# Kernel tuning notes

Hardware: AMD Instinct MI355X
Metric: run time of the kernel (lower is better)

Reference implementation:

```python
import jax, jax.numpy as jnp
import numpy as np

N = 100000      # nodes
F_IN = 500      # input features
HEADS = 8
HID = 8         # per-head hidden channels
NC = 16         # num classes
E = 1600000     # edges (avg degree 16)


def setup_inputs() -> dict:
    key = jax.random.key(0)
    ks = jax.random.split(key, 12)
    s = 0.1
    return {
        "x": jax.random.normal(ks[0], (N, F_IN), jnp.float32),
        "edge_index": jax.random.randint(ks[1], (2, E), 0, N, dtype=jnp.int64),
        "W1": jax.random.normal(ks[2], (F_IN, HEADS * HID), jnp.float32) * s,
        "a1_src": jax.random.normal(ks[3], (HEADS, HID), jnp.float32) * s,
        "a1_dst": jax.random.normal(ks[4], (HEADS, HID), jnp.float32) * s,
        "b1": jnp.zeros((HEADS * HID,), jnp.float32),
        "W2": jax.random.normal(ks[5], (HEADS * HID, NC), jnp.float32) * s,
        "a2_src": jax.random.normal(ks[6], (1, NC), jnp.float32) * s,
        "a2_dst": jax.random.normal(ks[7], (1, NC), jnp.float32) * s,
        "b2": jnp.zeros((NC,), jnp.float32),
        "Wg": jax.random.normal(ks[8], (NC, NC), jnp.float32) * s,
        "bg": jnp.zeros((NC,), jnp.float32),
    }


def _gat_layer(x, src, dst, W, a_src, a_dst, b, heads, ch):
    # PyG GATConv (eval mode): per-edge additive attention + scatter softmax.
    n = x.shape[0]
    h = (x @ W).reshape(n, heads, ch)                       # [N,H,C]
    al_s = jnp.einsum('nhc,hc->nh', h, a_src)               # [N,H]
    al_d = jnp.einsum('nhc,hc->nh', h, a_dst)
    e = jax.nn.leaky_relu(al_s[src] + al_d[dst], 0.2)       # [Etot,H]
    e_max = jax.ops.segment_max(e, dst, num_segments=n)     # stable softmax per dst
    ex = jnp.exp(e - e_max[dst])
    denom = jax.ops.segment_sum(ex, dst, num_segments=n)
    alpha = ex / (denom[dst] + 1e-16)                       # [Etot,H]
    out = jax.ops.segment_sum(alpha[:, :, None] * h[src], dst, num_segments=n)
    return out.reshape(n, heads * ch) + b


def _gcn_layer(x, src, dst, W, b):
    n = x.shape[0]
    deg = jax.ops.segment_sum(jnp.ones_like(dst, x.dtype), dst, num_segments=n)
    dinv = jnp.where(deg > 0, jax.lax.rsqrt(deg), 0.0)
    norm = dinv[src] * dinv[dst]                            # [Etot]
    xw = x @ W
    return jax.ops.segment_sum(norm[:, None] * xw[src], dst, num_segments=n) + b


def reference(x, edge_index, W1, a1_src, a1_dst, b1, W2, a2_src, a2_dst, b2, Wg, bg):
    n = x.shape[0]
    loop = jnp.arange(n, dtype=edge_index.dtype)
    src = jnp.concatenate([edge_index[0], loop])            # add self-loops (PyG default)
    dst = jnp.concatenate([edge_index[1], loop])
    # GAT: dropout layers are eval-mode no-ops
    h = jax.nn.elu(_gat_layer(x, src, dst, W1, a1_src, a1_dst, b1, HEADS, HID))
    h = _gat_layer(h, src, dst, W2, a2_src, a2_dst, b2, 1, NC)
    h = jax.nn.relu(h)                                      # activate='relu'
    return _gcn_layer(h, src, dst, Wg, bg)
```

## Files before the change

### kernel.cpp

```cpp
#include <hip/hip_runtime.h>
#include <hip/hip_bf16.h>
#include <math.h>

#define NNODES 100000
#define F_IN   500
#define HEADS  8
#define HID    8
#define NC     16

__global__ void zero_int_kernel(int* __restrict__ p, int n) {
    int i = blockIdx.x * blockDim.x + threadIdx.x;
    if (i < n) p[i] = 0;
}

__global__ void deg_kernel(const int* __restrict__ ei_dst, int* __restrict__ deg,
                           int E, int N) {
    int e = blockIdx.x * blockDim.x + threadIdx.x;
    int tot = E + N;
    if (e >= tot) return;
    int d = (e < E) ? ei_dst[e] : (e - E);
    atomicAdd(&deg[d], 1);
}

__global__ void scan1_kernel(const int* __restrict__ deg, int* __restrict__ bsum, int n) {
    __shared__ int s[256];
    int i = blockIdx.x * 256 + threadIdx.x;
    s[threadIdx.x] = (i < n) ? deg[i] : 0;
    __syncthreads();
    for (int off = 128; off > 0; off >>= 1) {
        if (threadIdx.x < off) s[threadIdx.x] += s[threadIdx.x + off];
        __syncthreads();
    }
    if (threadIdx.x == 0) bsum[blockIdx.x] = s[0];
}

__global__ void scan2_kernel(const int* __restrict__ bsum, int* __restrict__ bexcl, int nb) {
    __shared__ int s[512];
    int t = threadIdx.x;
    int orig = (t < nb) ? bsum[t] : 0;
    s[t] = orig;
    __syncthreads();
    for (int off = 1; off < 512; off <<= 1) {
        int v = (t >= off) ? s[t - off] : 0;
        __syncthreads();
        s[t] += v;
        __syncthreads();
    }
    if (t < nb) bexcl[t] = s[t] - orig;
}

__global__ void scan3_kernel(const int* __restrict__ deg, const int* __restrict__ bexcl,
                             int* __restrict__ rowptr, int n) {
    __shared__ int s[256];
    int t = threadIdx.x;
    int i = blockIdx.x * 256 + t;
    int v = (i < n) ? deg[i] : 0;
    s[t] = v;
    __syncthreads();
    for (int off = 1; off < 256; off <<= 1) {
        int u = (t >= off) ? s[t - off] : 0;
        __syncthreads();
        s[t] += u;
        __syncthreads();
    }
    if (i < n) rowptr[i + 1] = bexcl[blockIdx.x] + s[t];
    if (i == 0) rowptr[0] = 0;
}

__global__ void fill_kernel(const int* __restrict__ ei_src, const int* __restrict__ ei_dst,
                            const int* __restrict__ rowptr, int* __restrict__ cursor,
                            int* __restrict__ col, int E, int N) {
    int e = blockIdx.x * blockDim.x + threadIdx.x;
    int tot = E + N;
    if (e >= tot) return;
    int s, d;
    if (e < E) { s = ei_src[e]; d = ei_dst[e]; }
    else       { s = e - E;     d = s; }
    int pos = atomicAdd(&cursor[d], 1);
    col[rowptr[d] + pos] = s;
}

__global__ __launch_bounds__(256) void gemm1_kernel(const float* __restrict__ x,
                                                    const float* __restrict__ W,
                                                    float* __restrict__ h, int n) {
    __shared__ float xs[64][20];
    __shared__ float ws[20][64];
    int row0 = blockIdx.x * 64;
    int t = threadIdx.x;
    int ty = t >> 4, tx = t & 15;
    float acc[4][4] = {};
    for (int k0 = 0; k0 < F_IN; k0 += 20) {
#pragma unroll
        for (int i = 0; i < 5; ++i) {
            int f = t + i * 256;
            int r = f / 20, c = f - r * 20;
            int gr = row0 + r;
            xs[r][c] = (gr < n) ? x[(size_t)gr * F_IN + k0 + c] : 0.f;
        }
#pragma unroll
        for (int i = 0; i < 5; ++i) {
            int f = t + i * 256;
            int r = f >> 6, c = f & 63;
            ws[r][c] = W[(k0 + r) * 64 + c];
        }
        __syncthreads();
#pragma unroll
        for (int k = 0; k < 20; ++k) {
            float a[4], b[4];
#pragma unroll
            for (int i = 0; i < 4; ++i) a[i] = xs[ty * 4 + i][k];
#pragma unroll
            for (int j = 0; j < 4; ++j) b[j] = ws[k][tx * 4 + j];
#pragma unroll
            for (int i = 0; i < 4; ++i)
#pragma unroll
                for (int j = 0; j < 4; ++j) acc[i][j] += a[i] * b[j];
        }
        __syncthreads();
    }
#pragma unroll
    for (int i = 0; i < 4; ++i) {
        int gr = row0 + ty * 4 + i;
        if (gr < n) {
            float4 v = make_float4(acc[i][0], acc[i][1], acc[i][2], acc[i][3]);
            *reinterpret_cast<float4*>(h + (size_t)gr * 64 + tx * 4) = v;
        }
    }
}

__global__ void proj_al1_kernel(const float* __restrict__ h, const float* __restrict__ a1s,
                                const float* __restrict__ a1d, float* __restrict__ als,
                                float* __restrict__ ald, int n) {
    int nid = blockIdx.x * blockDim.x + threadIdx.x;
    if (nid >= n) return;
    const float* hp = h + (size_t)nid * 64;
#pragma unroll
    for (int hd = 0; hd < 8; ++hd) {
        float s = 0.f, d = 0.f;
#pragma unroll
        for (int c = 0; c < 8; ++c) {
            float hv = hp[hd * 8 + c];
            s += hv * a1s[hd * 8 + c];
            d += hv * a1d[hd * 8 + c];
        }
        als[nid * 8 + hd] = s;
        ald[nid * 8 + hd] = d;
    }
}

__global__ void gat1_edge_kernel(const int* __restrict__ rowptr, const int* __restrict__ col,
                                 const float* __restrict__ als, const float* __restrict__ ald,
                                 const float* __restrict__ h, const float* __restrict__ b1,
                                 float* __restrict__ out1, int n) {
    int tid = blockIdx.x * blockDim.x + threadIdx.x;
    int dst = tid >> 3, hd = tid & 7;
    if (dst >= n) return;
    int beg = rowptr[dst], end = rowptr[dst + 1];
    float ad = ald[dst * 8 + hd];
    float acc[8] = {};
    float den = 0.f;
    for (int j = beg; j < end; ++j) {
        int s = col[j];
        float e = als[s * 8 + hd] + ad;
        e = e > 0.f ? e : 0.2f * e;
        float w = expf(e);
        den += w;
        const float4* hp = reinterpret_cast<const float4*>(h + (size_t)s * 64 + hd * 8);
        float4 v0 = hp[0], v1 = hp[1];
        acc[0] += w * v0.x; acc[1] += w * v0.y; acc[2] += w * v0.z; acc[3] += w * v0.w;
        acc[4] += w * v1.x; acc[5] += w * v1.y; acc[6] += w * v1.z; acc[7] += w * v1.w;
    }
    float inv = 1.f / (den + 1e-16f);
#pragma unroll
    for (int c = 0; c < 8; ++c) {
        float v = acc[c] * inv + b1[hd * 8 + c];
        v = (v > 0.f) ? v : expm1f(v);
        out1[(size_t)dst * 64 + hd * 8 + c] = v;
    }
}

__global__ void proj2_kernel(const float* __restrict__ out1, const float* __restrict__ W2,
                             const float* __restrict__ a2s, const float* __restrict__ a2d,
                             float* __restrict__ h2, float* __restrict__ al2s,
                             float* __restrict__ al2d, int n) {
    int nid = blockIdx.x * blockDim.x + threadIdx.x;
    if (nid >= n) return;
    const float* op = out1 + (size_t)nid * 64;
    float acc[16] = {};
#pragma unroll 8
    for (int k = 0; k < 64; ++k) {
        float o = op[k];
#pragma unroll
        for (int c = 0; c < 16; ++c) acc[c] += o * W2[k * 16 + c];
    }
    float s = 0.f, d = 0.f;
#pragma unroll
    for (int c = 0; c < 16; ++c) {
        s += acc[c] * a2s[c];
        d += acc[c] * a2d[c];
        h2[(size_t)nid * 16 + c] = acc[c];
    }
    al2s[nid] = s;
    al2d[nid] = d;
}

__global__ void gat2_edge_kernel(const int* __restrict__ rowptr, const int* __restrict__ col,
                                 const float* __restrict__ al2s, const float* __restrict__ al2d,
                                 const float* __restrict__ h2, const float* __restrict__ b2,
                                 const float* __restrict__ Wg, float* __restrict__ xw,
                                 float* __restrict__ dinv, int n) {
    int dst = blockIdx.x * blockDim.x + threadIdx.x;
    if (dst >= n) return;
    int beg = rowptr[dst], end = rowptr[dst + 1];
    float ad = al2d[dst];
    float acc[16] = {};
    float den = 0.f;
    for (int j = beg; j < end; ++j) {
        int s = col[j];
        float e = al2s[s] + ad;
        e = e > 0.f ? e : 0.2f * e;
        float w = expf(e);
        den += w;
        const float4* hp = reinterpret_cast<const float4*>(h2 + (size_t)s * 16);
        float4 v0 = hp[0], v1 = hp[1], v2 = hp[2], v3 = hp[3];
        acc[0]  += w * v0.x; acc[1]  += w * v0.y; acc[2]  += w * v0.z; acc[3]  += w * v0.w;
        acc[4]  += w * v1.x; acc[5]  += w * v1.y; acc[6]  += w * v1.z; acc[7]  += w * v1.w;
        acc[8]  += w * v2.x; acc[9]  += w * v2.y; acc[10] += w * v2.z; acc[11] += w * v2.w;
        acc[12] += w * v3.x; acc[13] += w * v3.y; acc[14] += w * v3.z; acc[15] += w * v3.w;
    }
    float inv = 1.f / (den + 1e-16f);
    float r[16];
#pragma unroll
    for (int c = 0; c < 16; ++c) {
        float v = acc[c] * inv + b2[c];
        r[c] = (v > 0.f) ? v : 0.f;
    }
#pragma unroll
    for (int cp = 0; cp < 16; ++cp) {
        float s2 = 0.f;
#pragma unroll
        for (int c = 0; c < 16; ++c) s2 += r[c] * Wg[c * 16 + cp];
        xw[(size_t)dst * 16 + cp] = s2;
    }
    dinv[dst] = 1.f / sqrtf((float)(end - beg));
}

__global__ void gcn_kernel(const int* __restrict__ rowptr, const int* __restrict__ col,
                           const float* __restrict__ xw, const float* __restrict__ dinv,
                           const float* __restrict__ bg, float* __restrict__ out, int n) {
    int dst = blockIdx.x * blockDim.x + threadIdx.x;
    if (dst >= n) return;
    int beg = rowptr[dst], end = rowptr[dst + 1];
    float di = dinv[dst];
    float acc[16] = {};
    for (int j = beg; j < end; ++j) {
        int s = col[j];
        float nm = dinv[s] * di;
        const float4* xp = reinterpret_cast<const float4*>(xw + (size_t)s * 16);
        float4 v0 = xp[0], v1 = xp[1], v2 = xp[2], v3 = xp[3];
        acc[0]  += nm * v0.x; acc[1]  += nm * v0.y; acc[2]  += nm * v0.z; acc[3]  += nm * v0.w;
        acc[4]  += nm * v1.x; acc[5]  += nm * v1.y; acc[6]  += nm * v1.z; acc[7]  += nm * v1.w;
        acc[8]  += nm * v2.x; acc[9]  += nm * v2.y; acc[10] += nm * v2.z; acc[11] += nm * v2.w;
        acc[12] += nm * v3.x; acc[13] += nm * v3.y; acc[14] += nm * v3.z; acc[15] += nm * v3.w;
    }
#pragma unroll
    for (int c = 0; c < 16; ++c)
        out[(size_t)dst * 16 + c] = acc[c] + bg[c];
}

extern "C" void kernel_launch(void* const* d_in, const int* in_sizes, int n_in,
                              void* d_out, int out_size, void* d_ws, size_t ws_size,
                              hipStream_t stream) {
    const float* x    = (const float*)d_in[0];
    const int*   ei   = (const int*)d_in[1];
    const float* W1   = (const float*)d_in[2];
    const float* a1s  = (const float*)d_in[3];
    const float* a1d  = (const float*)d_in[4];
    const float* b1   = (const float*)d_in[5];
    const float* W2   = (const float*)d_in[6];
    const float* a2s  = (const float*)d_in[7];
    const float* a2d  = (const float*)d_in[8];
    const float* b2   = (const float*)d_in[9];
    const float* Wg   = (const float*)d_in[10];
    const float* bg   = (const float*)d_in[11];
    float* out = (float*)d_out;

    const int N = in_sizes[0] / F_IN;
    const int E = in_sizes[1] / 2;
    const int Etot = E + N;

    char* base = (char*)d_ws;
    size_t off = 0;
    auto alloc = [&](size_t bytes) -> char* {
        char* p = base + off;
        off = (off + bytes + 255) & ~(size_t)255;
        return p;
    };
    float* h    = (float*)alloc((size_t)N * 64 * 4);
    float* als  = (float*)alloc((size_t)N * 8 * 4);
    float* ald  = (float*)alloc((size_t)N * 8 * 4);
    float* out1 = (float*)alloc((size_t)N * 64 * 4);
    float* h2   = (float*)alloc((size_t)N * 16 * 4);
    float* al2s = (float*)alloc((size_t)N * 4);
    float* al2d = (float*)alloc((size_t)N * 4);
    float* xw   = (float*)alloc((size_t)N * 16 * 4);
    float* dinv = (float*)alloc((size_t)N * 4);
    int*   deg  = (int*)alloc((size_t)N * 4);
    int*   cur  = (int*)alloc((size_t)N * 4);
    int*   rowptr = (int*)alloc((size_t)(N + 1) * 4);
    int*   bsum = (int*)alloc(512 * 4);
    int*   bexcl= (int*)alloc(512 * 4);
    int*   col  = (int*)alloc((size_t)Etot * 4);

    const int* ei_src = ei;
    const int* ei_dst = ei + E;

    const int TB = 256;
    int nbN  = (N + TB - 1) / TB;
    int nbE  = (Etot + TB - 1) / TB;
    int nbG  = (N + 63) / 64;
    int nbA  = (N * 8 + TB - 1) / TB;

    zero_int_kernel<<<nbN, TB, 0, stream>>>(deg, N);
    zero_int_kernel<<<nbN, TB, 0, stream>>>(cur, N);
    deg_kernel<<<nbE, TB, 0, stream>>>(ei_dst, deg, E, N);
    scan1_kernel<<<nbN, TB, 0, stream>>>(deg, bsum, N);
    scan2_kernel<<<1, 512, 0, stream>>>(bsum, bexcl, nbN);
    scan3_kernel<<<nbN, TB, 0, stream>>>(deg, bexcl, rowptr, N);
    fill_kernel<<<nbE, TB, 0, stream>>>(ei_src, ei_dst, rowptr, cur, col, E, N);

    gemm1_kernel<<<nbG, TB, 0, stream>>>(x, W1, h, N);
    proj_al1_kernel<<<nbN, TB, 0, stream>>>(h, a1s, a1d, als, ald, N);
    gat1_edge_kernel<<<nbA, TB, 0, stream>>>(rowptr, col, als, ald, h, b1, out1, N);
    proj2_kernel<<<nbN, TB, 0, stream>>>(out1, W2, a2s, a2d, h2, al2s, al2d, N);
    gat2_edge_kernel<<<nbN, TB, 0, stream>>>(rowptr, col, al2s, al2d, h2, b2, Wg, xw, dinv, N);
    gcn_kernel<<<nbN, TB, 0, stream>>>(rowptr, col, xw, dinv, bg, out, N);
}
```

Measured before the change: 766.7 us.

## Run first-layer GEMM on MFMA with split-bf16 emulation of fp32

New measurement: 686.2 us. 1.12x faster.

```diff
diff --git a/kernel.cpp b/kernel.cpp
--- a/kernel.cpp
+++ b/kernel.cpp
@@ -4,9 +4,23 @@
 
 #define NNODES 100000
 #define F_IN   500
+#define KPAD   512
 #define HEADS  8
 #define HID    8
 #define NC     16
+
+typedef __attribute__((ext_vector_type(8))) short bf16x8;
+typedef __attribute__((ext_vector_type(4))) float f32x4;
+typedef __attribute__((ext_vector_type(8))) unsigned short u16x8;
+
+__device__ inline unsigned short f2bf_rne(float f) {
+    unsigned u = __float_as_uint(f);
+    u += 0x7FFF + ((u >> 16) & 1);
+    return (unsigned short)(u >> 16);
+}
+__device__ inline float bf2f(unsigned short h) {
+    return __uint_as_float(((unsigned)h) << 16);
+}
 
 __global__ void zero_int_kernel(int* __restrict__ p, int n) {
     int i = blockIdx.x * blockDim.x + threadIdx.x;
@@ -80,50 +94,134 @@
     col[rowptr[d] + pos] = s;
 }
 
-__global__ __launch_bounds__(256) void gemm1_kernel(const float* __restrict__ x,
-                                                    const float* __restrict__ W,
-                                                    float* __restrict__ h, int n) {
-    __shared__ float xs[64][20];
-    __shared__ float ws[20][64];
-    int row0 = blockIdx.x * 64;
+__global__ void transposeW1_kernel(const float* __restrict__ W, float* __restrict__ Wt) {
+    int i = blockIdx.x * blockDim.x + threadIdx.x;
+    if (i >= 64 * KPAD) return;
+    int c = i >> 9;
+    int k = i & (KPAD - 1);
+    Wt[i] = (k < F_IN) ? W[k * 64 + c] : 0.f;
+}
+
+#define BM  128
+#define BK  32
+#define LDT 40
+
+__global__ __launch_bounds__(256) void gemm1_mfma_kernel(
+        const float* __restrict__ x, const float* __restrict__ Wt,
+        float* __restrict__ h, int n) {
+    __shared__ unsigned short sAh[BM * LDT];
+    __shared__ unsigned short sAl[BM * LDT];
+    __shared__ unsigned short sBh[64 * LDT];
+    __shared__ unsigned short sBl[64 * LDT];
+
     int t = threadIdx.x;
-    int ty = t >> 4, tx = t & 15;
-    float acc[4][4] = {};
-    for (int k0 = 0; k0 < F_IN; k0 += 20) {
-#pragma unroll
-        for (int i = 0; i < 5; ++i) {
-            int f = t + i * 256;
-            int r = f / 20, c = f - r * 20;
-            int gr = row0 + r;
-            xs[r][c] = (gr < n) ? x[(size_t)gr * F_IN + k0 + c] : 0.f;
-        }
-#pragma unroll
-        for (int i = 0; i < 5; ++i) {
-            int f = t + i * 256;
-            int r = f >> 6, c = f & 63;
-            ws[r][c] = W[(k0 + r) * 64 + c];
-        }
-        __syncthreads();
-#pragma unroll
-        for (int k = 0; k < 20; ++k) {
-            float a[4], b[4];
-#pragma unroll
-            for (int i = 0; i < 4; ++i) a[i] = xs[ty * 4 + i][k];
-#pragma unroll
-            for (int j = 0; j < 4; ++j) b[j] = ws[k][tx * 4 + j];
-#pragma unroll
-            for (int i = 0; i < 4; ++i)
-#pragma unroll
-                for (int j = 0; j < 4; ++j) acc[i][j] += a[i] * b[j];
-        }
-        __syncthreads();
-    }
-#pragma unroll
-    for (int i = 0; i < 4; ++i) {
-        int gr = row0 + ty * 4 + i;
+    int wave = t >> 6, lane = t & 63;
+    int l15 = lane & 15, kgrp = lane >> 4;
+    int row0 = blockIdx.x * BM;
+    int wrow0 = wave * 32;
+
+    int ar = t >> 1;
+    int ak = (t & 1) * 16;
+    int bc = t >> 2;
+    int bk = (t & 3) * 8;
+
+    f32x4 acc[2][4];
+#pragma unroll
+    for (int m = 0; m < 2; ++m)
+#pragma unroll
+        for (int nn = 0; nn < 4; ++nn)
+            acc[m][nn] = (f32x4){0.f, 0.f, 0.f, 0.f};
+
+    const int gr = row0 + ar;
+
+    for (int k0 = 0; k0 < KPAD; k0 += BK) {
+        float av[16];
         if (gr < n) {
-            float4 v = make_float4(acc[i][0], acc[i][1], acc[i][2], acc[i][3]);
-            *reinterpret_cast<float4*>(h + (size_t)gr * 64 + tx * 4) = v;
+            if (k0 + BK <= F_IN) {
+                const float4* p = (const float4*)(x + (size_t)gr * F_IN + k0 + ak);
+                float4 q0 = p[0], q1 = p[1], q2 = p[2], q3 = p[3];
+                av[0]=q0.x; av[1]=q0.y; av[2]=q0.z; av[3]=q0.w;
+                av[4]=q1.x; av[5]=q1.y; av[6]=q1.z; av[7]=q1.w;
+                av[8]=q2.x; av[9]=q2.y; av[10]=q2.z; av[11]=q2.w;
+                av[12]=q3.x; av[13]=q3.y; av[14]=q3.z; av[15]=q3.w;
+            } else {
+#pragma unroll
+                for (int j = 0; j < 16; ++j) {
+                    int kk = k0 + ak + j;
+                    av[j] = (kk < F_IN) ? x[(size_t)gr * F_IN + kk] : 0.f;
+                }
+            }
+        } else {
+#pragma unroll
+            for (int j = 0; j < 16; ++j) av[j] = 0.f;
+        }
+        u16x8 ah0, ah1, al0, al1;
+#pragma unroll
+        for (int j = 0; j < 8; ++j) {
+            unsigned short hi = f2bf_rne(av[j]);
+            ah0[j] = hi;
+            al0[j] = f2bf_rne(av[j] - bf2f(hi));
+        }
+#pragma unroll
+        for (int j = 0; j < 8; ++j) {
+            unsigned short hi = f2bf_rne(av[8 + j]);
+            ah1[j] = hi;
+            al1[j] = f2bf_rne(av[8 + j] - bf2f(hi));
+        }
+        *(u16x8*)&sAh[ar * LDT + ak]     = ah0;
+        *(u16x8*)&sAh[ar * LDT + ak + 8] = ah1;
+        *(u16x8*)&sAl[ar * LDT + ak]     = al0;
+        *(u16x8*)&sAl[ar * LDT + ak + 8] = al1;
+
+        const float4* bp = (const float4*)(Wt + (size_t)bc * KPAD + k0 + bk);
+        float4 w0 = bp[0], w1 = bp[1];
+        float bv[8] = {w0.x, w0.y, w0.z, w0.w, w1.x, w1.y, w1.z, w1.w};
+        u16x8 bh, bl;
+#pragma unroll
+        for (int j = 0; j < 8; ++j) {
+            unsigned short hi = f2bf_rne(bv[j]);
+            bh[j] = hi;
+            bl[j] = f2bf_rne(bv[j] - bf2f(hi));
+        }
+        *(u16x8*)&sBh[bc * LDT + bk] = bh;
+        *(u16x8*)&sBl[bc * LDT + bk] = bl;
+
+        __syncthreads();
+
+        bf16x8 aH[2], aL[2], bH[4], bL[4];
+#pragma unroll
+        for (int m = 0; m < 2; ++m) {
+            int r = wrow0 + m * 16 + l15;
+            aH[m] = *(const bf16x8*)&sAh[r * LDT + kgrp * 8];
+            aL[m] = *(const bf16x8*)&sAl[r * LDT + kgrp * 8];
+        }
+#pragma unroll
+        for (int nn = 0; nn < 4; ++nn) {
+            int c = nn * 16 + l15;
+            bH[nn] = *(const bf16x8*)&sBh[c * LDT + kgrp * 8];
+            bL[nn] = *(const bf16x8*)&sBl[c * LDT + kgrp * 8];
+        }
+#pragma unroll
+        for (int m = 0; m < 2; ++m)
+#pragma unroll
+            for (int nn = 0; nn < 4; ++nn) {
+                acc[m][nn] = __builtin_amdgcn_mfma_f32_16x16x32_bf16(aH[m], bH[nn], acc[m][nn], 0, 0, 0);
+                acc[m][nn] = __builtin_amdgcn_mfma_f32_16x16x32_bf16(aH[m], bL[nn], acc[m][nn], 0, 0, 0);
+                acc[m][nn] = __builtin_amdgcn_mfma_f32_16x16x32_bf16(aL[m], bH[nn], acc[m][nn], 0, 0, 0);
+            }
+        __syncthreads();
+    }
+
+#pragma unroll
+    for (int m = 0; m < 2; ++m) {
+#pragma unroll
+        for (int nn = 0; nn < 4; ++nn) {
+#pragma unroll
+            for (int r = 0; r < 4; ++r) {
+                int row = row0 + wrow0 + m * 16 + kgrp * 4 + r;
+                if (row < n)
+                    h[(size_t)row * 64 + nn * 16 + l15] = acc[m][nn][r];
+            }
         }
     }
 }
@@ -311,6 +409,7 @@
     int*   bsum = (int*)alloc(512 * 4);
     int*   bexcl= (int*)alloc(512 * 4);
     int*   col  = (int*)alloc((size_t)Etot * 4);
+    float* Wt   = (float*)alloc((size_t)64 * KPAD * 4);
 
     const int* ei_src = ei;
     const int* ei_dst = ei + E;
@@ -318,7 +417,7 @@
     const int TB = 256;
     int nbN  = (N + TB - 1) / TB;
     int nbE  = (Etot + TB - 1) / TB;
-    int nbG  = (N + 63) / 64;
+    int nbG  = (N + BM - 1) / BM;
     int nbA  = (N * 8 + TB - 1) / TB;
 
     zero_int_kernel<<<nbN, TB, 0, stream>>>(deg, N);
@@ -329,7 +428,8 @@
     scan3_kernel<<<nbN, TB, 0, stream>>>(deg, bexcl, rowptr, N);
     fill_kernel<<<nbE, TB, 0, stream>>>(ei_src, ei_dst, rowptr, cur, col, E, N);
 
-    gemm1_kernel<<<nbG, TB, 0, stream>>>(x, W1, h, N);
+    transposeW1_kernel<<<(64 * KPAD + TB - 1) / TB, TB, 0, stream>>>(W1, Wt);
+    gemm1_mfma_kernel<<<nbG, TB, 0, stream>>>(x, Wt, h, N);
     proj_al1_kernel<<<nbN, TB, 0, stream>>>(h, a1s, a1d, als, ald, N);
     gat1_edge_kernel<<<nbA, TB, 0, stream>>>(rowptr, col, als, ald, h, b1, out1, N);
     proj2_kernel<<<nbN, TB, 0, stream>>>(out1, W2, a2s, a2d, h2, al2s, al2d, N);
```
